# Kernel tuning notes

Hardware: AMD Instinct MI355X
Metric: run time of the kernel (lower is better)

The kernel has to match this reference:

```python
import jax, jax.numpy as jnp
import numpy as np

B, H, S, D = 4, 16, 2048, 64

def setup_inputs() -> dict:
    key = jax.random.key(0)
    kq, kk, kv = jax.random.split(key, 3)
    q = jax.random.normal(kq, (B, H, S, D), dtype=jnp.float32)
    k = jax.random.normal(kk, (B, H, S, D), dtype=jnp.float32)
    v = jax.random.normal(kv, (B, H, S, D), dtype=jnp.float32)
    return {"q": q, "k": k, "v": v}

def reference(q, k, v):
    # Based linear attention: Taylor-expanded exp kernel, causal, row-sum normalized.
    d = q.shape[-1]
    scale = 1.0 / jnp.sqrt(jnp.asarray(d, dtype=q.dtype))
    s = jnp.einsum('bhqd,bhkd->bhqk', q, k) * scale          # [B,H,S,S]
    p = 1.0 + s + 0.5 * (s * s)                               # Taylor exp approx
    seq = s.shape[-1]
    causal = jnp.tril(jnp.ones((seq, seq), dtype=bool))       # [S,S]
    p = jnp.where(causal, p, 0.0)
    denom = jnp.sum(p, axis=-1, keepdims=True) + 1e-6         # [B,H,S,1]
    out = jnp.einsum('bhqk,bhkd->bhqd', p, v) / denom
    return out
```

## Files before the change

### kernel.cpp

```cpp
#include <hip/hip_runtime.h>
#include <hip/hip_bf16.h>

#define S_LEN 2048
#define DH    64
#define QB    128
#define KB    64
#define BHN   64
#define NQT   16
#define LDS_STRIDE 72

typedef __attribute__((ext_vector_type(8))) short short8;
typedef __attribute__((ext_vector_type(4))) float f32x4;

union Frag {
  short8   s;
  unsigned u[4];
};

__device__ __forceinline__ unsigned pack2(float a, float b) {
  __hip_bfloat162 h2 = __float22bfloat162_rn(make_float2(a, b));
  unsigned u; __builtin_memcpy(&u, &h2, 4);
  return u;
}

__global__ __launch_bounds__(256, 2)
void repack(const float* __restrict__ Kg, const float* __restrict__ Vg,
            short* __restrict__ ws) {
  const int bt = blockIdx.x;
  const int tid = threadIdx.x;
  const size_t tilebase = (size_t)bt * (64 * 64);
  short* kout = ws + (size_t)bt * 4096;
  short* vout = ws + 8388608 + (size_t)bt * 4096;

#pragma unroll
  for (int it = 0; it < 2; ++it) {
    const int c2 = tid + it * 256;
    const int f = c2 >> 6, l = c2 & 63;
    const int kkh = f >> 2, hi = (f >> 1) & 1, cc = f & 1;
    const int row = kkh * 32 + hi * 16 + (l & 15);
    const int col = cc * 32 + (l >> 4) * 8;
    const float* src = Kg + tilebase + row * 64 + col;
    float4 a = *(const float4*)src, b = *(const float4*)(src + 4);
    Frag w;
    w.u[0] = pack2(a.x, a.y); w.u[1] = pack2(a.z, a.w);
    w.u[2] = pack2(b.x, b.y); w.u[3] = pack2(b.z, b.w);
    *(short8*)(kout + f * 512 + l * 8) = w.s;
  }

  __shared__ float vt[64 * 65];
#pragma unroll
  for (int it = 0; it < 4; ++it) {
    const int i = tid + it * 256;
    const int r = i >> 4, c4 = i & 15;
    float4 x = *(const float4*)(Vg + tilebase + r * 64 + c4 * 4);
    vt[r * 65 + c4 * 4 + 0] = x.x; vt[r * 65 + c4 * 4 + 1] = x.y;
    vt[r * 65 + c4 * 4 + 2] = x.z; vt[r * 65 + c4 * 4 + 3] = x.w;
  }
  __syncthreads();
#pragma unroll
  for (int it = 0; it < 2; ++it) {
    const int v2 = tid + it * 256;
    const int v = v2 >> 6, l = v2 & 63;
    const int kkh = v >> 2, n = v & 3;
    const int d = n * 16 + (l & 15);
    const int k0c = kkh * 32 + (l >> 4) * 8;
    Frag w;
#pragma unroll
    for (int jj = 0; jj < 4; ++jj)
      w.u[jj] = pack2(vt[(k0c + 2 * jj) * 65 + d], vt[(k0c + 2 * jj + 1) * 65 + d]);
    *(short8*)(vout + v * 512 + l * 8) = w.s;
  }
}

#define GLOAD2(t_, T0, T1, T2, T3)                                             \
  do {                                                                         \
    const short* g_ = gk + (size_t)(t_) * 4096;                                \
    T0 = *(const short8*)(g_ + 0 * 512);                                       \
    T1 = *(const short8*)(g_ + 1 * 512);                                       \
    T2 = *(const short8*)(g_ + 2 * 512);                                       \
    T3 = *(const short8*)(g_ + 3 * 512);                                       \
  } while (0)

#define DSWRITE2(t_, T0, T1, T2, T3)                                           \
  do {                                                                         \
    short* w_ = wr + ((t_) & 1) * 8192;                                        \
    *(short8*)(w_ + 0 * 512) = T0;                                             \
    *(short8*)(w_ + 1 * 512) = T1;                                             \
    *(short8*)(w_ + 2 * 512) = T2;                                             \
    *(short8*)(w_ + 3 * 512) = T3;                                             \
  } while (0)

#define PHASE(t_, MASKED_)                                                     \
  do {                                                                         \
    const short* rd_ = rd + ((t_) & 1) * 8192;                                 \
    const int k0_ = (t_) * KB;                                                 \
    _Pragma("unroll")                                                          \
    for (int kkh = 0; kkh < 2; ++kkh) {                                        \
      const int kk = kkh * 32;                                                 \
      if (!(MASKED_) || (q0 + wv * 32 + 31 >= k0_ + kk)) {                     \
        short8 kf[4], vf[4];                                                   \
        _Pragma("unroll")                                                      \
        for (int j = 0; j < 4; ++j) {                                          \
          kf[j] = *(const short8*)(rd_ + (kkh * 4 + j) * 512);                 \
          vf[j] = *(const short8*)(rd_ + 4096 + (kkh * 4 + j) * 512);          \
        }                                                                      \
        f32x4 stL[2], stH[2];                                                  \
        _Pragma("unroll")                                                      \
        for (int hq = 0; hq < 2; ++hq) {                                       \
          stL[hq] = onesf;                                                     \
          stH[hq] = onesf;                                                     \
          _Pragma("unroll")                                                    \
          for (int c = 0; c < 2; ++c) {                                        \
            stL[hq] = __builtin_amdgcn_mfma_f32_16x16x32_bf16(kf[c],     qf[hq][c].s, stL[hq], 0, 0, 0); \
            stH[hq] = __builtin_amdgcn_mfma_f32_16x16x32_bf16(kf[2 + c], qf[hq][c].s, stH[hq], 0, 0, 0); \
          }                                                                    \
        }                                                                      \
        unsigned wrd[2][4];                                                    \
        _Pragma("unroll")                                                      \
        for (int hq = 0; hq < 2; ++hq) {                                       \
          const int qrow = q0 + wv * 32 + hq * 16 + qid;                       \
          float pl[4], ph[4];                                                  \
          _Pragma("unroll")                                                    \
          for (int r = 0; r < 4; ++r) {                                        \
            float tl = stL[hq][r], th = stH[hq][r];                            \
            pl[r] = fmaf(tl, tl, 1.0f);             \
            ph[r] = fmaf(th, th, 1.0f);                                        \
            if (MASKED_) {                                                     \
              if (k0_ + kk + 4 * g + r > qrow)      pl[r] = 0.f;               \
              if (k0_ + kk + 16 + 4 * g + r > qrow) ph[r] = 0.f;               \
            }                                                                  \
          }                                                                    \
          wrd[hq][0] = pack2(pl[0], pl[1]);                                    \
          wrd[hq][1] = pack2(pl[2], pl[3]);                                    \
          wrd[hq][2] = pack2(ph[0], ph[1]);                                    \
          wrd[hq][3] = pack2(ph[2], ph[3]);                                    \
        }                                                                      \
        Frag pa[2];                                                            \
        _Pragma("unroll")                                                      \
        for (int hq = 0; hq < 2; ++hq) {                                       \
          auto sA32 = __builtin_amdgcn_permlane32_swap(wrd[hq][0], wrd[hq][2], false, false); \
          auto sA16 = __builtin_amdgcn_permlane16_swap(sA32[0], sA32[1], false, false);       \
          auto sB32 = __builtin_amdgcn_permlane32_swap(wrd[hq][1], wrd[hq][3], false, false); \
          auto sB16 = __builtin_amdgcn_permlane16_swap(sB32[0], sB32[1], false, false);       \
          pa[hq].u[0] = (unsigned)sA16[0];                                     \
          pa[hq].u[2] = (unsigned)sA16[1];                                     \
          pa[hq].u[1] = (unsigned)sB16[0];                                     \
          pa[hq].u[3] = (unsigned)sB16[1];                                     \
        }                                                                      \
        _Pragma("unroll")                                                      \
        for (int n = 0; n < 4; ++n) {                                          \
          acc[0][n] = __builtin_amdgcn_mfma_f32_16x16x32_bf16(pa[0].s, vf[n], acc[0][n], 0, 0, 0); \
          acc[1][n] = __builtin_amdgcn_mfma_f32_16x16x32_bf16(pa[1].s, vf[n], acc[1][n], 0, 0, 0); \
        }                                                                      \
        dacc[0] = __builtin_amdgcn_mfma_f32_16x16x32_bf16(pa[0].s, ones.s, dacc[0], 0, 0, 0); \
        dacc[1] = __builtin_amdgcn_mfma_f32_16x16x32_bf16(pa[1].s, ones.s, dacc[1], 0, 0, 0); \
      }                                                                        \
    }                                                                          \
  } while (0)

__global__ __launch_bounds__(256, 4)
void based_one(const float* __restrict__ Qg, const short* __restrict__ Fr,
               float* __restrict__ Og) {
  const int tid  = threadIdx.x;
  const int lane = tid & 63;
  const int wv   = tid >> 6;
  const int qid  = lane & 15;
  const int g    = lane >> 4;

  const int bh = blockIdx.x;
  const int qt = NQT - 1 - (int)blockIdx.y;
  const int q0 = qt * QB;

  __shared__ __align__(16) short ring[2 * 8192];

  const size_t base = (size_t)bh * S_LEN;

  const short* gk = Fr + ((wv < 2) ? 0 : 8388608)
                    + ((size_t)(bh << 5) << 12) + (wv & 1) * 2048 + lane * 8;
  short* wr = &ring[((wv >= 2) ? 4096 : 0) + (wv & 1) * 2048 + lane * 8];
  const short* rd = &ring[lane * 8];

  Frag ones;
  {
    const unsigned ov = (qid == 0) ? 0x3F803F80u : 0u;
    ones.u[0] = ov; ones.u[1] = ov; ones.u[2] = ov; ones.u[3] = ov;
  }
  const f32x4 onesf = (f32x4){1.f, 1.f, 1.f, 1.f};

  Frag qf[2][2];
  {
    const float SC = 0.125f;
#pragma unroll
    for (int hq = 0; hq < 2; ++hq) {
      const int qrow = q0 + wv * 32 + hq * 16 + qid;
      const float* qp = Qg + (base + qrow) * DH + g * 8;
#pragma unroll
      for (int c = 0; c < 2; ++c) {
        float4 f0 = *(const float4*)(qp + c * 32);
        float4 f1 = *(const float4*)(qp + c * 32 + 4);
        qf[hq][c].u[0] = pack2(f0.x * SC, f0.y * SC);
        qf[hq][c].u[1] = pack2(f0.z * SC, f0.w * SC);
        qf[hq][c].u[2] = pack2(f1.x * SC, f1.y * SC);
        qf[hq][c].u[3] = pack2(f1.z * SC, f1.w * SC);
      }
    }
  }

  f32x4 acc[2][4];
  f32x4 dacc[2];
#pragma unroll
  for (int hq = 0; hq < 2; ++hq) {
    dacc[hq] = (f32x4){0.f, 0.f, 0.f, 0.f};
#pragma unroll
    for (int n = 0; n < 4; ++n) acc[hq][n] = (f32x4){0.f, 0.f, 0.f, 0.f};
  }

  const int nfull = 2 * qt;

  short8 a0, a1, a2, a3;

  GLOAD2(0, a0, a1, a2, a3);
  DSWRITE2(0, a0, a1, a2, a3);
  __syncthreads();

  for (int t = 0; t < nfull; ++t) {
    GLOAD2(t + 1, a0, a1, a2, a3);
    PHASE(t, 0);
    DSWRITE2(t + 1, a0, a1, a2, a3);
    __syncthreads();
  }
  GLOAD2(nfull + 1, a0, a1, a2, a3);
  PHASE(nfull, 1);
  DSWRITE2(nfull + 1, a0, a1, a2, a3);
  __syncthreads();
  PHASE(nfull + 1, 1);

#pragma unroll
  for (int hq = 0; hq < 2; ++hq) {
#pragma unroll
    for (int r = 0; r < 4; ++r) {
      float dn  = __shfl(dacc[hq][r], 16 * g);
      float inv = 1.0f / (dn + 2e-6f);
      const int row = q0 + wv * 32 + hq * 16 + 4 * g + r;
      float* op = Og + (base + row) * DH + qid;
#pragma unroll
      for (int n = 0; n < 4; ++n) op[n * 16] = acc[hq][n][r] * inv;
    }
  }
}

#define STAGE_LOAD(k0_)                                                        \
  do {                                                                         \
    if (tid < 128) {                                                           \
      const float4* ksrc = (const float4*)(Kg + (base + (size_t)(k0_)) * DH); \
      r0 = ksrc[tid];       r1 = ksrc[tid + 128];                              \
      r2 = ksrc[tid + 256]; r3 = ksrc[tid + 384];                              \
      r4 = ksrc[tid + 512]; r5 = ksrc[tid + 640];                              \
      r6 = ksrc[tid + 768]; r7 = ksrc[tid + 896];                              \
    } else {                                                                   \
      const float4* vsrc = (const float4*)(Vg + (base + (size_t)(k0_)) * DH)  \
                           + ((tid - 128) >> 4) * 128 + ((tid - 128) & 15);    \
      r0 = vsrc[0];  r1 = vsrc[16]; r2 = vsrc[32]; r3 = vsrc[48];              \
      r4 = vsrc[64]; r5 = vsrc[80]; r6 = vsrc[96]; r7 = vsrc[112];             \
    }                                                                          \
  } while (0)

#define STAGE_WRITE(b_)                                                        \
  do {                                                                         \
    if (tid < 128) {                                                           \
      short* Kd = Klds[b_];                                                    \
      const int rb = tid >> 4, c4 = tid & 15;                                  \
      *(uint2*)&Kd[(rb + 0)  * LDS_STRIDE + c4 * 4] = make_uint2(pack2(r0.x, r0.y), pack2(r0.z, r0.w)); \
      *(uint2*)&Kd[(rb + 8)  * LDS_STRIDE + c4 * 4] = make_uint2(pack2(r1.x, r1.y), pack2(r1.z, r1.w)); \
      *(uint2*)&Kd[(rb + 16) * LDS_STRIDE + c4 * 4] = make_uint2(pack2(r2.x, r2.y), pack2(r2.z, r2.w)); \
      *(uint2*)&Kd[(rb + 24) * LDS_STRIDE + c4 * 4] = make_uint2(pack2(r3.x, r3.y), pack2(r3.z, r3.w)); \
      *(uint2*)&Kd[(rb + 32) * LDS_STRIDE + c4 * 4] = make_uint2(pack2(r4.x, r4.y), pack2(r4.z, r4.w)); \
      *(uint2*)&Kd[(rb + 40) * LDS_STRIDE + c4 * 4] = make_uint2(pack2(r5.x, r5.y), pack2(r5.z, r5.w)); \
      *(uint2*)&Kd[(rb + 48) * LDS_STRIDE + c4 * 4] = make_uint2(pack2(r6.x, r6.y), pack2(r6.z, r6.w)); \
      *(uint2*)&Kd[(rb + 56) * LDS_STRIDE + c4 * 4] = make_uint2(pack2(r7.x, r7.y), pack2(r7.z, r7.w)); \
    } else {                                                                   \
      short* Vd = Vlds[b_];                                                    \
      const int l = tid - 128, c4 = l & 15, rp = l >> 4;                       \
      const int slot = (rp + (c4 & 7)) & 7;                                    \
      short* vp = &Vd[(c4 * 4) * LDS_STRIDE + slot * 8];                       \
      Frag w;                                                                  \
      w.u[0] = pack2(r0.x, r1.x); w.u[1] = pack2(r2.x, r3.x);                  \
      w.u[2] = pack2(r4.x, r5.x); w.u[3] = pack2(r6.x, r7.x);                  \
      *(short8*)&vp[0 * LDS_STRIDE] = w.s;                                     \
      w.u[0] = pack2(r0.y, r1.y); w.u[1] = pack2(r2.y, r3.y);                  \
      w.u[2] = pack2(r4.y, r5.y); w.u[3] = pack2(r6.y, r7.y);                  \
      *(short8*)&vp[1 * LDS_STRIDE] = w.s;                                     \
      w.u[0] = pack2(r0.z, r1.z); w.u[1] = pack2(r2.z, r3.z);                  \
      w.u[2] = pack2(r4.z, r5.z); w.u[3] = pack2(r6.z, r7.z);                  \
      *(short8*)&vp[2 * LDS_STRIDE] = w.s;                                     \
      w.u[0] = pack2(r0.w, r1.w); w.u[1] = pack2(r2.w, r3.w);                  \
      w.u[2] = pack2(r4.w, r5.w); w.u[3] = pack2(r6.w, r7.w);                  \
      *(short8*)&vp[3 * LDS_STRIDE] = w.s;                                     \
    }                                                                          \
  } while (0)

#define COMPUTE_TILE(KbP_, VbP_, k0_, MASKED_)                                 \
  do {                                                                         \
    const short* Kb = (KbP_);                                                  \
    const short* Vb = (VbP_);                                                  \
    _Pragma("unroll")                                                          \
    for (int kk = 0; kk < KB; kk += 32) {                                      \
      if (!(MASKED_) || (q0 + wv * 32 + 31 >= (k0_) + kk)) {                   \
        short8 aLo[2], aHi[2];                                                 \
        _Pragma("unroll")                                                      \
        for (int c = 0; c < 2; ++c) {                                          \
          aLo[c] = *(const short8*)&Kb[(kk + qid) * LDS_STRIDE + c * 32 + g * 8];        \
          aHi[c] = *(const short8*)&Kb[(kk + 16 + qid) * LDS_STRIDE + c * 32 + g * 8];   \
        }                                                                      \
        f32x4 stL[2], stH[2];                                                  \
        _Pragma("unroll")                                                      \
        for (int hq = 0; hq < 2; ++hq) {                                       \
          stL[hq] = (f32x4){0.f, 0.f, 0.f, 0.f};                               \
          stH[hq] = (f32x4){0.f, 0.f, 0.f, 0.f};                               \
          _Pragma("unroll")                                                    \
          for (int c = 0; c < 2; ++c) {                                        \
            stL[hq] = __builtin_amdgcn_mfma_f32_16x16x32_bf16(aLo[c], qf[hq][c].s, stL[hq], 0, 0, 0); \
            stH[hq] = __builtin_amdgcn_mfma_f32_16x16x32_bf16(aHi[c], qf[hq][c].s, stH[hq], 0, 0, 0); \
          }                                                                    \
        }                                                                      \
        unsigned wrd[2][4];                                                    \
        _Pragma("unroll")                                                      \
        for (int hq = 0; hq < 2; ++hq) {                                       \
          const int qrow = q0 + wv * 32 + hq * 16 + qid;                       \
          float pl[4], ph[4];                                                  \
          _Pragma("unroll")                                                    \
          for (int r = 0; r < 4; ++r) {                                        \
            float sl = stL[hq][r], sh = stH[hq][r];                            \
            pl[r] = fmaf(sl, fmaf(sl, 0.5f, 1.0f), 1.0f);                      \
            ph[r] = fmaf(sh, fmaf(sh, 0.5f, 1.0f), 1.0f);                      \
            if (MASKED_) {                                                     \
              if ((k0_) + kk + 4 * g + r > qrow)      pl[r] = 0.f;             \
              if ((k0_) + kk + 16 + 4 * g + r > qrow) ph[r] = 0.f;             \
            }                                                                  \
          }                                                                    \
          wrd[hq][0] = pack2(pl[0], pl[1]);                                    \
          wrd[hq][1] = pack2(pl[2], pl[3]);                                    \
          wrd[hq][2] = pack2(ph[0], ph[1]);                                    \
          wrd[hq][3] = pack2(ph[2], ph[3]);                                    \
        }                                                                      \
        Frag pa[2];                                                            \
        _Pragma("unroll")                                                      \
        for (int hq = 0; hq < 2; ++hq) {                                       \
          auto sA32 = __builtin_amdgcn_permlane32_swap(wrd[hq][0], wrd[hq][2], false, false); \
          auto sA16 = __builtin_amdgcn_permlane16_swap(sA32[0], sA32[1], false, false);       \
          auto sB32 = __builtin_amdgcn_permlane32_swap(wrd[hq][1], wrd[hq][3], false, false); \
          auto sB16 = __builtin_amdgcn_permlane16_swap(sB32[0], sB32[1], false, false);       \
          pa[hq].u[0] = (unsigned)sA16[0];                                     \
          pa[hq].u[2] = (unsigned)sA16[1];                                     \
          pa[hq].u[1] = (unsigned)sB16[0];                                     \
          pa[hq].u[3] = (unsigned)sB16[1];                                     \
        }                                                                      \
        _Pragma("unroll")                                                      \
        for (int n = 0; n < 4; ++n) {                                          \
          const int row = n * 16 + qid;                                        \
          const int un  = ((kk >> 3) + g + ((row >> 2) & 7)) & 7;              \
          short8 vb = *(const short8*)&Vb[row * LDS_STRIDE + un * 8];          \
          acc[0][n] = __builtin_amdgcn_mfma_f32_16x16x32_bf16(pa[0].s, vb, acc[0][n], 0, 0, 0); \
          acc[1][n] = __builtin_amdgcn_mfma_f32_16x16x32_bf16(pa[1].s, vb, acc[1][n], 0, 0, 0); \
        }                                                                      \
        dacc[0] = __builtin_amdgcn_mfma_f32_16x16x32_bf16(pa[0].s, ones.s, dacc[0], 0, 0, 0);   \
        dacc[1] = __builtin_amdgcn_mfma_f32_16x16x32_bf16(pa[1].s, ones.s, dacc[1], 0, 0, 0);   \
      }                                                                        \
    }                                                                          \
  } while (0)

__global__ __launch_bounds__(256, 2)
void based_attn(const float* __restrict__ Qg,
                const float* __restrict__ Kg,
                const float* __restrict__ Vg,
                float* __restrict__ Og) {
  const int tid  = threadIdx.x;
  const int lane = tid & 63;
  const int wv   = tid >> 6;
  const int qid  = lane & 15;
  const int g    = lane >> 4;

  const int bh = blockIdx.x;
  const int qy = blockIdx.y;

  __shared__ short Klds[2][KB * LDS_STRIDE];
  __shared__ short Vlds[2][DH * LDS_STRIDE];

  const size_t base = (size_t)bh * S_LEN;

  Frag ones;
  {
    const unsigned ov = (qid == 0) ? 0x3F803F80u : 0u;
    ones.u[0] = ov; ones.u[1] = ov; ones.u[2] = ov; ones.u[3] = ov;
  }

  float4 r0, r1, r2, r3, r4, r5, r6, r7;

#pragma unroll 1
  for (int half = 0; half < 2; ++half) {
    const int qt = half ? (NQT - 1 - qy) : qy;
    const int q0 = qt * QB;

    Frag qf[2][2];
    {
      const float SC = 0.125f;
#pragma unroll
      for (int hq = 0; hq < 2; ++hq) {
        const int qrow = q0 + wv * 32 + hq * 16 + qid;
        const float* qp = Qg + (base + qrow) * DH + g * 8;
#pragma unroll
        for (int c = 0; c < 2; ++c) {
          float4 f0 = *(const float4*)(qp + c * 32);
          float4 f1 = *(const float4*)(qp + c * 32 + 4);
          qf[hq][c].u[0] = pack2(f0.x * SC, f0.y * SC);
          qf[hq][c].u[1] = pack2(f0.z * SC, f0.w * SC);
          qf[hq][c].u[2] = pack2(f1.x * SC, f1.y * SC);
          qf[hq][c].u[3] = pack2(f1.z * SC, f1.w * SC);
        }
      }
    }

    f32x4 acc[2][4];
    f32x4 dacc[2];
#pragma unroll
    for (int hq = 0; hq < 2; ++hq) {
      dacc[hq] = (f32x4){0.f, 0.f, 0.f, 0.f};
#pragma unroll
      for (int n = 0; n < 4; ++n) acc[hq][n] = (f32x4){0.f, 0.f, 0.f, 0.f};
    }

    STAGE_LOAD(0);
    STAGE_WRITE(0);
    __syncthreads();

    const int nfull = 2 * qt;
    for (int t = 0; t < nfull; ++t) {
      STAGE_LOAD((t + 1) * KB);
      COMPUTE_TILE(Klds[t & 1], Vlds[t & 1], t * KB, 0);
      STAGE_WRITE((t + 1) & 1);
      __syncthreads();
    }
    {
      int t = nfull;
      STAGE_LOAD((t + 1) * KB);
      COMPUTE_TILE(Klds[t & 1], Vlds[t & 1], t * KB, 1);
      STAGE_WRITE((t + 1) & 1);
      __syncthreads();
      t = nfull + 1;
      COMPUTE_TILE(Klds[t & 1], Vlds[t & 1], t * KB, 1);
    }

#pragma unroll
    for (int hq = 0; hq < 2; ++hq) {
#pragma unroll
      for (int r = 0; r < 4; ++r) {
        float dn  = __shfl(dacc[hq][r], 16 * g);
        float inv = 1.0f / (dn + 1e-6f);
        const int row = q0 + wv * 32 + hq * 16 + 4 * g + r;
        float* op = Og + (base + row) * DH + qid;
#pragma unroll
        for (int n = 0; n < 4; ++n) op[n * 16] = acc[hq][n][r] * inv;
      }
    }
  }
}

extern "C" void kernel_launch(void* const* d_in, const int* in_sizes, int n_in,
                              void* d_out, int out_size, void* d_ws, size_t ws_size,
                              hipStream_t stream) {
  (void)in_sizes; (void)n_in; (void)out_size;
  const float* Q = (const float*)d_in[0];
  const float* K = (const float*)d_in[1];
  const float* V = (const float*)d_in[2];
  float* O = (float*)d_out;

  if (ws_size >= (size_t)33554432) {
    short* ws = (short*)d_ws;
    repack<<<dim3(2048), 256, 0, stream>>>(K, V, ws);
    based_one<<<dim3(64, 16), 256, 0, stream>>>(Q, ws, O);
  } else {
    dim3 grid(BHN, NQT / 2);
    based_attn<<<grid, 256, 0, stream>>>(Q, K, V, O);
  }
}
```

Measured before the change: 64.52 us.

## Triple-buffer K/V ring with two-deep prefetch and MFMA priority hints

```diff
diff --git a/kernel.cpp b/kernel.cpp
--- a/kernel.cpp
+++ b/kernel.cpp
@@ -72,7 +72,7 @@
   }
 }
 
-#define GLOAD2(t_, T0, T1, T2, T3)                                             \
+#define GLOAD3(t_, T0, T1, T2, T3)                                             \
   do {                                                                         \
     const short* g_ = gk + (size_t)(t_) * 4096;                                \
     T0 = *(const short8*)(g_ + 0 * 512);                                       \
@@ -81,18 +81,18 @@
     T3 = *(const short8*)(g_ + 3 * 512);                                       \
   } while (0)
 
-#define DSWRITE2(t_, T0, T1, T2, T3)                                           \
-  do {                                                                         \
-    short* w_ = wr + ((t_) & 1) * 8192;                                        \
+#define DSWRITE3(slot_, T0, T1, T2, T3)                                        \
+  do {                                                                         \
+    short* w_ = wr + (slot_) * 8192;                                           \
     *(short8*)(w_ + 0 * 512) = T0;                                             \
     *(short8*)(w_ + 1 * 512) = T1;                                             \
     *(short8*)(w_ + 2 * 512) = T2;                                             \
     *(short8*)(w_ + 3 * 512) = T3;                                             \
   } while (0)
 
-#define PHASE(t_, MASKED_)                                                     \
-  do {                                                                         \
-    const short* rd_ = rd + ((t_) & 1) * 8192;                                 \
+#define PHASE(t_, slot_, MASKED_)                                              \
+  do {                                                                         \
+    const short* rd_ = rd + (slot_) * 8192;                                    \
     const int k0_ = (t_) * KB;                                                 \
     _Pragma("unroll")                                                          \
     for (int kkh = 0; kkh < 2; ++kkh) {                                        \
@@ -105,6 +105,7 @@
           vf[j] = *(const short8*)(rd_ + 4096 + (kkh * 4 + j) * 512);          \
         }                                                                      \
         f32x4 stL[2], stH[2];                                                  \
+        __builtin_amdgcn_s_setprio(1);                                         \
         _Pragma("unroll")                                                      \
         for (int hq = 0; hq < 2; ++hq) {                                       \
           stL[hq] = onesf;                                                     \
@@ -115,6 +116,7 @@
             stH[hq] = __builtin_amdgcn_mfma_f32_16x16x32_bf16(kf[2 + c], qf[hq][c].s, stH[hq], 0, 0, 0); \
           }                                                                    \
         }                                                                      \
+        __builtin_amdgcn_s_setprio(0);                                         \
         unsigned wrd[2][4];                                                    \
         _Pragma("unroll")                                                      \
         for (int hq = 0; hq < 2; ++hq) {                                       \
@@ -147,6 +149,7 @@
           pa[hq].u[1] = (unsigned)sB16[0];                                     \
           pa[hq].u[3] = (unsigned)sB16[1];                                     \
         }                                                                      \
+        __builtin_amdgcn_s_setprio(1);                                         \
         _Pragma("unroll")                                                      \
         for (int n = 0; n < 4; ++n) {                                          \
           acc[0][n] = __builtin_amdgcn_mfma_f32_16x16x32_bf16(pa[0].s, vf[n], acc[0][n], 0, 0, 0); \
@@ -154,11 +157,12 @@
         }                                                                      \
         dacc[0] = __builtin_amdgcn_mfma_f32_16x16x32_bf16(pa[0].s, ones.s, dacc[0], 0, 0, 0); \
         dacc[1] = __builtin_amdgcn_mfma_f32_16x16x32_bf16(pa[1].s, ones.s, dacc[1], 0, 0, 0); \
+        __builtin_amdgcn_s_setprio(0);                                         \
       }                                                                        \
     }                                                                          \
   } while (0)
 
-__global__ __launch_bounds__(256, 4)
+__global__ __launch_bounds__(256, 3)
 void based_one(const float* __restrict__ Qg, const short* __restrict__ Fr,
                float* __restrict__ Og) {
   const int tid  = threadIdx.x;
@@ -171,7 +175,7 @@
   const int qt = NQT - 1 - (int)blockIdx.y;
   const int q0 = qt * QB;
 
-  __shared__ __align__(16) short ring[2 * 8192];
+  __shared__ __align__(16) short ring[3 * 8192];
 
   const size_t base = (size_t)bh * S_LEN;
 
@@ -218,22 +222,31 @@
   const int nfull = 2 * qt;
 
   short8 a0, a1, a2, a3;
-
-  GLOAD2(0, a0, a1, a2, a3);
-  DSWRITE2(0, a0, a1, a2, a3);
+  short8 b0, b1, b2, b3;
+
+  GLOAD3(0, a0, a1, a2, a3);
+  DSWRITE3(0, a0, a1, a2, a3);
+  GLOAD3(1, a0, a1, a2, a3);
+  DSWRITE3(1, a0, a1, a2, a3);
+  if (nfull > 0) GLOAD3(2, a0, a1, a2, a3);
   __syncthreads();
 
-  for (int t = 0; t < nfull; ++t) {
-    GLOAD2(t + 1, a0, a1, a2, a3);
-    PHASE(t, 0);
-    DSWRITE2(t + 1, a0, a1, a2, a3);
+  int sA = 0, sB = 1, sC = 2;
+  for (int t = 0; t < nfull; t += 2) {
+    const bool lB = (t + 3 <= nfull + 1);
+    if (lB) GLOAD3(t + 3, b0, b1, b2, b3);
+    PHASE(t, sA, 0);
+    DSWRITE3(sC, a0, a1, a2, a3);
     __syncthreads();
-  }
-  GLOAD2(nfull + 1, a0, a1, a2, a3);
-  PHASE(nfull, 1);
-  DSWRITE2(nfull + 1, a0, a1, a2, a3);
-  __syncthreads();
-  PHASE(nfull + 1, 1);
+    const bool lA = (t + 4 <= nfull + 1);
+    if (lA) GLOAD3(t + 4, a0, a1, a2, a3);
+    PHASE(t + 1, sB, 0);
+    if (lB) DSWRITE3(sA, b0, b1, b2, b3);
+    __syncthreads();
+    const int tmp = sC; sC = sB; sB = sA; sA = tmp;
+  }
+  PHASE(nfull, sA, 1);
+  PHASE(nfull + 1, sB, 1);
 
 #pragma unroll
   for (int hq = 0; hq < 2; ++hq) {
```

Measured after the change: 66.30 us. +2.8%, slower.
